# Optimization experiments

Measured on AMD Instinct MI355X. Metric: run time of the kernel, lower is better.

The kernel has to match this reference:

```python
import jax, jax.numpy as jnp
import numpy as np

B = 128      # args.batch_size
E = 256      # args.num_embed
M = 64       # per-sample positions per embedding channel
S = 3        # number of scales == conv kernel width
C = 5        # args.classes
SCALES = [4, 8, 16]
EPS = 1e-5


def _rnn_last(x, wih, whh, bih, bhh):
    """Elman RNN with input/hidden size 1 over x:(N,T,1); returns last hidden (N,)."""
    xT = jnp.transpose(x[:, :, 0])  # (T, N)
    def step(h, xt):
        h = jnp.tanh(xt * wih + bih + h * whh + bhh)
        return h, None
    h0 = jnp.zeros((x.shape[0],), x.dtype)
    hT, _ = jax.lax.scan(step, h0, xT)
    return hT


def setup_inputs() -> dict:
    key = jax.random.key(0)
    ks = jax.random.split(key, 20)
    N = B * M * E
    inp = {}
    for i, T in enumerate(SCALES):
        inp[f"a{i}"] = jax.random.normal(ks[i], (N, T, 1), dtype=jnp.float32)
    sc = 0.5
    inp["rnn1_wih"] = sc * jax.random.normal(ks[3], (S,), dtype=jnp.float32)
    inp["rnn1_whh"] = sc * jax.random.normal(ks[4], (S,), dtype=jnp.float32)
    inp["rnn1_bih"] = sc * jax.random.normal(ks[5], (S,), dtype=jnp.float32)
    inp["rnn1_bhh"] = sc * jax.random.normal(ks[6], (S,), dtype=jnp.float32)
    inp["conv_w"] = sc * jax.random.normal(ks[7], (S,), dtype=jnp.float32)
    inp["conv_b"] = sc * jax.random.normal(ks[8], (1,), dtype=jnp.float32)
    inp["rnn2_wih"] = sc * jax.random.normal(ks[9], (1,), dtype=jnp.float32)
    inp["rnn2_whh"] = sc * jax.random.normal(ks[10], (1,), dtype=jnp.float32)
    inp["rnn2_bih"] = sc * jax.random.normal(ks[11], (1,), dtype=jnp.float32)
    inp["rnn2_bhh"] = sc * jax.random.normal(ks[12], (1,), dtype=jnp.float32)
    inp["norm_gamma"] = jnp.ones((E,), dtype=jnp.float32)
    inp["norm_beta"] = jnp.zeros((E,), dtype=jnp.float32)
    inp["fnn_w"] = jax.random.normal(ks[13], (C, E), dtype=jnp.float32) / C
    inp["fnn_b"] = jnp.zeros((C,), dtype=jnp.float32)
    return inp


def reference(a0, a1, a2, rnn1_wih, rnn1_whh, rnn1_bih, rnn1_bhh,
              conv_w, conv_b, rnn2_wih, rnn2_whh, rnn2_bih, rnn2_bhh,
              norm_gamma, norm_beta, fnn_w, fnn_b):
    # per-scale scalar RNNs; keep last hidden state, reshape to (B, M, E, 1)
    rst = []
    for i, a in enumerate((a0, a1, a2)):
        h = _rnn_last(a, rnn1_wih[i], rnn1_whh[i], rnn1_bih[i], rnn1_bhh[i])
        rst.append(h.reshape(B, M, E, 1))
    c = jnp.concatenate(rst, axis=-1)          # (B, M, E, S)
    cp = jnp.transpose(c, (0, 2, 1, 3))        # (B, E, M, S)
    # Conv2d(1,1,(1,3)) over (M,S) with S==kernel width -> single output column
    fusion = jnp.einsum('bems,s->bem', cp, conv_w) + conv_b[0]  # (B, E, M)
    # second scalar RNN over the M axis for each (b, e) lane
    seq2 = fusion.reshape(B * E, M, 1)
    h2 = _rnn_last(seq2, rnn2_wih[0], rnn2_whh[0], rnn2_bih[0], rnn2_bhh[0])
    feat = h2.reshape(B, E)
    # BatchNorm1d (training-mode batch statistics, biased variance)
    mean = feat.mean(axis=0)
    var = feat.var(axis=0)
    xn = (feat - mean) / jnp.sqrt(var + EPS) * norm_gamma + norm_beta
    logits = jax.nn.relu(xn) @ fnn_w.T + fnn_b  # (B, C)
    return jax.nn.softmax(logits, axis=1)
```

## Files before the change

### kernel.cpp

```cpp
#include <hip/hip_runtime.h>
#include <math.h>

#define Bb 128
#define Ee 256
#define Mm 64
#define Cc 5
#define NTOT (Bb*Mm*Ee)
#define BE  (Bb*Ee)
#define EPS 1e-5f
#define L2E2 2.8853900817779268f

#if __has_builtin(__builtin_amdgcn_exp2f)
#define EXP2(x) __builtin_amdgcn_exp2f(x)
#else
#define EXP2(x) exp2f(x)
#endif
#define RCP(x) __builtin_amdgcn_rcpf(x)

__device__ __forceinline__ float tanh_step(float x, float w, float b, float u, float h) {
    float t = __builtin_fmaf(x, w, b);
    t = __builtin_fmaf(h, u, t);
    float r = RCP(EXP2(t) + 1.0f);
    return __builtin_fmaf(-2.0f, r, 1.0f);
}

__global__ __launch_bounds__(256) void k_rnn1(
    const float* __restrict__ a0, const float* __restrict__ a1,
    const float* __restrict__ a2,
    const float* __restrict__ wih, const float* __restrict__ whh,
    const float* __restrict__ bih, const float* __restrict__ bhh,
    const float* __restrict__ cw,  const float* __restrict__ cb,
    float* __restrict__ fusion)
{
    int t = blockIdx.x * blockDim.x + threadIdx.x;

    float w0 = wih[0] * L2E2, w1 = wih[1] * L2E2, w2 = wih[2] * L2E2;
    float u0 = whh[0] * L2E2, u1 = whh[1] * L2E2, u2 = whh[2] * L2E2;
    float b0 = (bih[0] + bhh[0]) * L2E2;
    float b1 = (bih[1] + bhh[1]) * L2E2;
    float b2 = (bih[2] + bhh[2]) * L2E2;
    float c0 = cw[0], c1 = cw[1], c2 = cw[2], cbias = cb[0];

    #pragma unroll
    for (int s = 0; s < 2; ++s) {
        int n = t + s * (NTOT / 2);

        float4 x0 = ((const float4*)a0)[n];
        float h0 = tanh_step(x0.x, w0, b0, u0, 0.0f);
        h0 = tanh_step(x0.y, w0, b0, u0, h0);
        h0 = tanh_step(x0.z, w0, b0, u0, h0);
        h0 = tanh_step(x0.w, w0, b0, u0, h0);

        float4 y0 = ((const float4*)a1)[2*n + 0];
        float4 y1 = ((const float4*)a1)[2*n + 1];
        float h1 = tanh_step(y0.x, w1, b1, u1, 0.0f);
        h1 = tanh_step(y0.y, w1, b1, u1, h1);
        h1 = tanh_step(y0.z, w1, b1, u1, h1);
        h1 = tanh_step(y0.w, w1, b1, u1, h1);
        h1 = tanh_step(y1.x, w1, b1, u1, h1);
        h1 = tanh_step(y1.y, w1, b1, u1, h1);
        h1 = tanh_step(y1.z, w1, b1, u1, h1);
        h1 = tanh_step(y1.w, w1, b1, u1, h1);

        float h2 = 0.0f;
        #pragma unroll
        for (int q = 0; q < 4; ++q) {
            float4 z = ((const float4*)a2)[4*n + q];
            h2 = tanh_step(z.x, w2, b2, u2, h2);
            h2 = tanh_step(z.y, w2, b2, u2, h2);
            h2 = tanh_step(z.z, w2, b2, u2, h2);
            h2 = tanh_step(z.w, w2, b2, u2, h2);
        }

        float f = h0 * c0 + h1 * c1 + h2 * c2 + cbias;

        int e = n & (Ee - 1);
        int m = (n >> 8) & (Mm - 1);
        int b = n >> 14;
        fusion[(m << 15) + (b << 8) + e] = f;
    }
}

__global__ __launch_bounds__(256) void k_rnn2(
    const float* __restrict__ fusion,
    const float* __restrict__ w, const float* __restrict__ u,
    const float* __restrict__ bi, const float* __restrict__ bh,
    float* __restrict__ feat)
{
    int j = blockIdx.x * blockDim.x + threadIdx.x;
    float wv = w[0] * L2E2, uv = u[0] * L2E2, bb = (bi[0] + bh[0]) * L2E2;
    float h = 0.0f;
    #pragma unroll 8
    for (int m = 0; m < Mm; ++m) {
        float x = fusion[m * BE + j];
        h = tanh_step(x, wv, bb, uv, h);
    }
    feat[j] = h;
}

__global__ __launch_bounds__(256) void k_stats(
    const float* __restrict__ feat,
    const float* __restrict__ gamma, const float* __restrict__ beta,
    float* __restrict__ scale, float* __restrict__ shift)
{
    int e = threadIdx.x;
    float s = 0.0f, s2 = 0.0f;
    for (int b = 0; b < Bb; ++b) {
        float v = feat[b * Ee + e];
        s  += v;
        s2 += v * v;
    }
    float mean = s * (1.0f / Bb);
    float var  = s2 * (1.0f / Bb) - mean * mean;
    float a = gamma[e] * rsqrtf(var + EPS);
    scale[e] = a;
    shift[e] = beta[e] - mean * a;
}

__global__ __launch_bounds__(256) void k_head(
    const float* __restrict__ feat,
    const float* __restrict__ scale, const float* __restrict__ shift,
    const float* __restrict__ fw, const float* __restrict__ fb,
    float* __restrict__ out)
{
    int b = blockIdx.x;
    int e = threadIdx.x;

    float v = feat[b * Ee + e] * scale[e] + shift[e];
    v = fmaxf(v, 0.0f);

    float p[Cc];
    #pragma unroll
    for (int c = 0; c < Cc; ++c) p[c] = v * fw[c * Ee + e];

    #pragma unroll
    for (int off = 32; off > 0; off >>= 1) {
        #pragma unroll
        for (int c = 0; c < Cc; ++c) p[c] += __shfl_down(p[c], off);
    }

    __shared__ float lds[4][Cc];
    int wave = e >> 6, lane = e & 63;
    if (lane == 0) {
        #pragma unroll
        for (int c = 0; c < Cc; ++c) lds[wave][c] = p[c];
    }
    __syncthreads();

    if (e == 0) {
        float lg[Cc];
        #pragma unroll
        for (int c = 0; c < Cc; ++c)
            lg[c] = lds[0][c] + lds[1][c] + lds[2][c] + lds[3][c] + fb[c];
        float mx = lg[0];
        #pragma unroll
        for (int c = 1; c < Cc; ++c) mx = fmaxf(mx, lg[c]);
        float se = 0.0f;
        #pragma unroll
        for (int c = 0; c < Cc; ++c) { lg[c] = EXP2((lg[c] - mx) * 1.4426950408889634f); se += lg[c]; }
        float inv = RCP(se);
        #pragma unroll
        for (int c = 0; c < Cc; ++c) out[b * Cc + c] = lg[c] * inv;
    }
}

extern "C" void kernel_launch(void* const* d_in, const int* in_sizes, int n_in,
                              void* d_out, int out_size, void* d_ws, size_t ws_size,
                              hipStream_t stream) {
    const float* a0       = (const float*)d_in[0];
    const float* a1       = (const float*)d_in[1];
    const float* a2       = (const float*)d_in[2];
    const float* rnn1_wih = (const float*)d_in[3];
    const float* rnn1_whh = (const float*)d_in[4];
    const float* rnn1_bih = (const float*)d_in[5];
    const float* rnn1_bhh = (const float*)d_in[6];
    const float* conv_w   = (const float*)d_in[7];
    const float* conv_b   = (const float*)d_in[8];
    const float* rnn2_wih = (const float*)d_in[9];
    const float* rnn2_whh = (const float*)d_in[10];
    const float* rnn2_bih = (const float*)d_in[11];
    const float* rnn2_bhh = (const float*)d_in[12];
    const float* gamma    = (const float*)d_in[13];
    const float* beta     = (const float*)d_in[14];
    const float* fnn_w    = (const float*)d_in[15];
    const float* fnn_b    = (const float*)d_in[16];

    float* out = (float*)d_out;

    char* ws = (char*)d_ws;
    float* fusion = (float*)ws;
    float* feat   = (float*)(ws + (size_t)Mm * BE * 4);
    float* scale  = feat + BE;
    float* shift  = scale + Ee;

    k_rnn1<<<NTOT / 2 / 256, 256, 0, stream>>>(a0, a1, a2,
        rnn1_wih, rnn1_whh, rnn1_bih, rnn1_bhh, conv_w, conv_b, fusion);
    k_rnn2<<<BE / 256, 256, 0, stream>>>(fusion,
        rnn2_wih, rnn2_whh, rnn2_bih, rnn2_bhh, feat);
    k_stats<<<1, 256, 0, stream>>>(feat, gamma, beta, scale, shift);
    k_head<<<Bb, 256, 0, stream>>>(feat, scale, shift, fnn_w, fnn_b, out);
}
```

Measured before the change: 52.08 us.

## Store fusion intermediate as bf16 and merge BatchNorm stats into head kernel

The intermediate fusion tensor is now written and read as bf16 instead of fp32, halving its global traffic between the two RNN kernels. The separate single-block stats kernel is removed, and every head block recomputes the per-channel mean and variance itself, saving one launch at the cost of redundant reads of feat. The change also adds an occupancy hint to k_rnn1's launch bounds and raises the unroll factor in k_rnn2. The bf16 rounding adds error that passes through the 64-step second RNN.

```diff
diff --git a/kernel.cpp b/kernel.cpp
--- a/kernel.cpp
+++ b/kernel.cpp
@@ -24,13 +24,22 @@
     return __builtin_fmaf(-2.0f, r, 1.0f);
 }
 
-__global__ __launch_bounds__(256) void k_rnn1(
+__device__ __forceinline__ unsigned short f32_to_bf16_rne(float f) {
+    unsigned u = __float_as_uint(f);
+    unsigned r = (u + 0x7fffu + ((u >> 16) & 1u)) >> 16;
+    return (unsigned short)r;
+}
+__device__ __forceinline__ float bf16_to_f32(unsigned short s) {
+    return __uint_as_float(((unsigned)s) << 16);
+}
+
+__global__ __launch_bounds__(256, 8) void k_rnn1(
     const float* __restrict__ a0, const float* __restrict__ a1,
     const float* __restrict__ a2,
     const float* __restrict__ wih, const float* __restrict__ whh,
     const float* __restrict__ bih, const float* __restrict__ bhh,
     const float* __restrict__ cw,  const float* __restrict__ cb,
-    float* __restrict__ fusion)
+    unsigned short* __restrict__ fusion)
 {
     int t = blockIdx.x * blockDim.x + threadIdx.x;
 
@@ -77,12 +86,12 @@
         int e = n & (Ee - 1);
         int m = (n >> 8) & (Mm - 1);
         int b = n >> 14;
-        fusion[(m << 15) + (b << 8) + e] = f;
+        fusion[(m << 15) + (b << 8) + e] = f32_to_bf16_rne(f);
     }
 }
 
 __global__ __launch_bounds__(256) void k_rnn2(
-    const float* __restrict__ fusion,
+    const unsigned short* __restrict__ fusion,
     const float* __restrict__ w, const float* __restrict__ u,
     const float* __restrict__ bi, const float* __restrict__ bh,
     float* __restrict__ feat)
@@ -90,43 +99,36 @@
     int j = blockIdx.x * blockDim.x + threadIdx.x;
     float wv = w[0] * L2E2, uv = u[0] * L2E2, bb = (bi[0] + bh[0]) * L2E2;
     float h = 0.0f;
-    #pragma unroll 8
+    #pragma unroll 16
     for (int m = 0; m < Mm; ++m) {
-        float x = fusion[m * BE + j];
+        float x = bf16_to_f32(fusion[m * BE + j]);
         h = tanh_step(x, wv, bb, uv, h);
     }
     feat[j] = h;
 }
 
-__global__ __launch_bounds__(256) void k_stats(
+__global__ __launch_bounds__(256) void k_head(
     const float* __restrict__ feat,
     const float* __restrict__ gamma, const float* __restrict__ beta,
-    float* __restrict__ scale, float* __restrict__ shift)
-{
-    int e = threadIdx.x;
-    float s = 0.0f, s2 = 0.0f;
-    for (int b = 0; b < Bb; ++b) {
-        float v = feat[b * Ee + e];
-        s  += v;
-        s2 += v * v;
-    }
-    float mean = s * (1.0f / Bb);
-    float var  = s2 * (1.0f / Bb) - mean * mean;
-    float a = gamma[e] * rsqrtf(var + EPS);
-    scale[e] = a;
-    shift[e] = beta[e] - mean * a;
-}
-
-__global__ __launch_bounds__(256) void k_head(
-    const float* __restrict__ feat,
-    const float* __restrict__ scale, const float* __restrict__ shift,
     const float* __restrict__ fw, const float* __restrict__ fb,
     float* __restrict__ out)
 {
     int b = blockIdx.x;
     int e = threadIdx.x;
 
-    float v = feat[b * Ee + e] * scale[e] + shift[e];
+    float s = 0.0f, s2 = 0.0f;
+    #pragma unroll 8
+    for (int bb = 0; bb < Bb; ++bb) {
+        float v = feat[bb * Ee + e];
+        s  += v;
+        s2 += v * v;
+    }
+    float mean = s * (1.0f / Bb);
+    float var  = s2 * (1.0f / Bb) - mean * mean;
+    float a = gamma[e] * rsqrtf(var + EPS);
+    float shift = beta[e] - mean * a;
+
+    float v = feat[b * Ee + e] * a + shift;
     v = fmaxf(v, 0.0f);
 
     float p[Cc];
@@ -188,15 +190,12 @@
     float* out = (float*)d_out;
 
     char* ws = (char*)d_ws;
-    float* fusion = (float*)ws;
-    float* feat   = (float*)(ws + (size_t)Mm * BE * 4);
-    float* scale  = feat + BE;
-    float* shift  = scale + Ee;
+    unsigned short* fusion = (unsigned short*)ws;
+    float* feat = (float*)(ws + (size_t)Mm * BE * 2);
 
     k_rnn1<<<NTOT / 2 / 256, 256, 0, stream>>>(a0, a1, a2,
         rnn1_wih, rnn1_whh, rnn1_bih, rnn1_bhh, conv_w, conv_b, fusion);
     k_rnn2<<<BE / 256, 256, 0, stream>>>(fusion,
         rnn2_wih, rnn2_whh, rnn2_bih, rnn2_bhh, feat);
-    k_stats<<<1, 256, 0, stream>>>(feat, gamma, beta, scale, shift);
-    k_head<<<Bb, 256, 0, stream>>>(feat, scale, shift, fnn_w, fnn_b, out);
-}
+    k_head<<<Bb, 256, 0, stream>>>(feat, gamma, beta, fnn_w, fnn_b, out);
+}
```

Result: faster. 50.81 us (-2.4%).
